# Kernel tuning notes

Hardware: AMD Instinct MI355X
Metric: run time of the kernel (lower is better)

Reference implementation:

```python
import jax, jax.numpy as jnp
import numpy as np

N_NODES = 100000
N_EDGES = 640000


def _sage_conv(x, src, dst, w_agg, b, w_root, n_nodes):
    # mean aggregation of source features into destination nodes
    msgs = x[src]  # [E, D] gather
    summed = jax.ops.segment_sum(msgs, dst, num_segments=n_nodes)  # [N, D]
    deg = jax.ops.segment_sum(jnp.ones((src.shape[0],), dtype=x.dtype), dst,
                              num_segments=n_nodes)  # [N]
    mean = summed / jnp.clip(deg, 1.0)[:, None]  # isolated nodes -> 0
    # PyG SAGEConv: lin_l(agg) + lin_r(x); bias lives on lin_l
    return mean @ w_agg.T + b + x @ w_root.T


def setup_inputs() -> dict:
    key = jax.random.key(0)
    ks = jax.random.split(key, 8)
    d_in, d_hid, d_out = 128, 256, 64
    x = jax.random.normal(ks[0], (N_NODES, d_in), dtype=jnp.float32)
    edge_index = jax.random.randint(ks[1], (2, N_EDGES), 0, N_NODES, dtype=jnp.int64)
    s = 0.05
    return {
        "x": x,
        "edge_index": edge_index,
        "w1_agg": jax.random.normal(ks[2], (d_hid, d_in), dtype=jnp.float32) * s,
        "b1": jax.random.normal(ks[3], (d_hid,), dtype=jnp.float32) * s,
        "w1_root": jax.random.normal(ks[4], (d_hid, d_in), dtype=jnp.float32) * s,
        "w2_agg": jax.random.normal(ks[5], (d_out, d_hid), dtype=jnp.float32) * s,
        "b2": jax.random.normal(ks[6], (d_out,), dtype=jnp.float32) * s,
        "w2_root": jax.random.normal(ks[7], (d_out, d_hid), dtype=jnp.float32) * s,
    }


def reference(x, edge_index, w1_agg, b1, w1_root, w2_agg, b2, w2_root):
    src, dst = edge_index[0], edge_index[1]
    n = x.shape[0]
    h = _sage_conv(x, src, dst, w1_agg, b1, w1_root, n)
    h = jax.nn.relu(h)
    # dropout(p=0.5) is identity in eval mode
    h = _sage_conv(h, src, dst, w2_agg, b2, w2_root, n)
    return jax.nn.log_softmax(h, axis=1)
```

## Files before the change

### kernel.cpp

```cpp
#include <hip/hip_runtime.h>

#define N_NODES 100000
#define N_EDGES 640000
#define D_IN 128
#define D_HID 256
#define D_OUT 64

#define NROWPAD 100096
#define CAP 32

#define OB_CNT      0u
#define OB_BUCKET   401408u
#define OB_XQ       13201408u
#define OB_MEANQ    26013696u
#define OB_HB       38825984u
#define OB_ZRB      90075136u
#define OB_ZAQ      102887424u
#define OB_WCAT1    109293568u
#define OB_WCAT2    109424640u

typedef __attribute__((ext_vector_type(8))) short bf16x8;
typedef __attribute__((ext_vector_type(4))) float f32x4;
typedef __attribute__((ext_vector_type(2))) float f32x2;

__device__ __forceinline__ ushort f2bf(float f) {
    uint u = __float_as_uint(f);
    u += 0x7FFFu + ((u >> 16) & 1u);
    return (ushort)(u >> 16);
}
__device__ __forceinline__ float bf1(ushort u) { return __uint_as_float((uint)u << 16); }
__device__ __forceinline__ uchar f2q(float v) {
    return (uchar)(__builtin_amdgcn_cvt_pk_fp8_f32(v, v, 0, false) & 0xFF);
}
__device__ __forceinline__ uint pk8(float4 v) {
    uint q = (uint)__builtin_amdgcn_cvt_pk_fp8_f32(v.x, v.y, 0, false);
    return (uint)__builtin_amdgcn_cvt_pk_fp8_f32(v.z, v.w, (int)q, true);
}
__device__ __forceinline__ uint pkbf(float lo, float hi) {
    return (__float_as_uint(lo) >> 16) | (__float_as_uint(hi) & 0xFFFF0000u);
}


__global__ __launch_bounds__(256) void k_z(
    int* __restrict__ cnt,
    const float* __restrict__ w1a, const float* __restrict__ w1r,
    const float* __restrict__ w2r, const float* __restrict__ w2a,
    ushort* __restrict__ wcat1, ushort* __restrict__ wcat2)
{
    int b = blockIdx.x;
    if (b < 98) {
        int i = (b * 256 + threadIdx.x) * 4;
        *(int4*)(cnt + i) = make_int4(0, 0, 0, 0);
    } else {
        int i = (b - 98) * 256 + threadIdx.x;
        if (i < 65536) {
            int n = i >> 8, k = i & 255;
            float v = (k < 128) ? w1a[n * 128 + k] : w1r[n * 128 + (k - 128)];
            wcat1[i] = f2bf(v);
        } else {
            int j = i - 65536;
            int n = j >> 8, k = j & 255;
            float v = (n < 64) ? w2r[n * 256 + k] : w2a[(n - 64) * 256 + k];
            wcat2[j] = f2bf(v);
        }
    }
}


__global__ __launch_bounds__(256) void k_fc(
    const int* __restrict__ src, const int* __restrict__ dst,
    int* __restrict__ cnt, int* __restrict__ bucket,
    const float* __restrict__ x, uchar* __restrict__ xq)
{
    int b = blockIdx.x;
    int tid = threadIdx.x;

    if (b < 625) {
        int e = (b * 256 + tid) * 4;
        int4 d = *(const int4*)(dst + e);
        int4 sv = *(const int4*)(src + e);
        int p0 = atomicAdd(&cnt[d.x], 1);
        int p1 = atomicAdd(&cnt[d.y], 1);
        int p2 = atomicAdd(&cnt[d.z], 1);
        int p3 = atomicAdd(&cnt[d.w], 1);

        size_t i = ((size_t)b * 256 + tid) * 16;
        float4 v0 = *(const float4*)(x + i);
        float4 v1 = *(const float4*)(x + i + 4);
        float4 v2 = *(const float4*)(x + i + 8);
        float4 v3 = *(const float4*)(x + i + 12);
        uint4 q;
        q.x = pk8(v0); q.y = pk8(v1); q.z = pk8(v2); q.w = pk8(v3);
        *(uint4*)(xq + i) = q;

        if (p0 < CAP) bucket[(d.x << 5) + p0] = sv.x;
        if (p1 < CAP) bucket[(d.y << 5) + p1] = sv.y;
        if (p2 < CAP) bucket[(d.z << 5) + p2] = sv.z;
        if (p3 < CAP) bucket[(d.w << 5) + p3] = sv.w;
    } else {
        size_t i = ((size_t)b * 256 + tid) * 16;
        float4 v0 = *(const float4*)(x + i);
        float4 v1 = *(const float4*)(x + i + 4);
        float4 v2 = *(const float4*)(x + i + 8);
        float4 v3 = *(const float4*)(x + i + 12);
        uint4 q;
        q.x = pk8(v0); q.y = pk8(v1); q.z = pk8(v2); q.w = pk8(v3);
        *(uint4*)(xq + i) = q;
    }
}


__global__ __launch_bounds__(256) void k_gather(
    const uchar* __restrict__ xq, const int* __restrict__ cnt,
    const int* __restrict__ bucket, uchar* __restrict__ meanq)
{
    int tid = threadIdx.x;
    int node = blockIdx.x * 8 + (tid >> 5);
    int l = tid & 31;
    int g = l & 3, t = l >> 2;
    int nraw = cnt[node];
    int n = min(nraw, CAP);
    const int* cs = bucket + (node << 5);

    float a[16] = {};
    for (int j = 0; j < n; j += 4) {
        int jj = j + g;
        int ii = (jj < n) ? jj : 0;
        float w = (jj < n) ? 1.0f : 0.0f;
        int s = cs[ii];
        uint4 q = *(const uint4*)(xq + (size_t)s * D_IN + t * 16);
        f32x2 p;
        p = __builtin_amdgcn_cvt_pk_f32_fp8(q.x, false); a[0] += w*p.x; a[1] += w*p.y;
        p = __builtin_amdgcn_cvt_pk_f32_fp8(q.x, true);  a[2] += w*p.x; a[3] += w*p.y;
        p = __builtin_amdgcn_cvt_pk_f32_fp8(q.y, false); a[4] += w*p.x; a[5] += w*p.y;
        p = __builtin_amdgcn_cvt_pk_f32_fp8(q.y, true);  a[6] += w*p.x; a[7] += w*p.y;
        p = __builtin_amdgcn_cvt_pk_f32_fp8(q.z, false); a[8] += w*p.x; a[9] += w*p.y;
        p = __builtin_amdgcn_cvt_pk_f32_fp8(q.z, true);  a[10]+= w*p.x; a[11]+= w*p.y;
        p = __builtin_amdgcn_cvt_pk_f32_fp8(q.w, false); a[12]+= w*p.x; a[13]+= w*p.y;
        p = __builtin_amdgcn_cvt_pk_f32_fp8(q.w, true);  a[14]+= w*p.x; a[15]+= w*p.y;
    }

    float b[8];
    #pragma unroll
    for (int j = 0; j < 8; ++j) {
        int base = (j & 3) + 8 * (j >> 2);
        float mine = (l & 1) ? a[base + 4] : a[base];
        float send = (l & 1) ? a[base]     : a[base + 4];
        b[j] = mine + __shfl_xor(send, 1);
    }
    float c[4];
    #pragma unroll
    for (int j = 0; j < 4; ++j) {
        float mine = (l & 2) ? b[j + 4] : b[j];
        float send = (l & 2) ? b[j]     : b[j + 4];
        c[j] = mine + __shfl_xor(send, 2);
    }
    float id = 1.0f / fmaxf((float)nraw, 1.0f);
    uint q = (uint)__builtin_amdgcn_cvt_pk_fp8_f32(c[0] * id, c[1] * id, 0, false);
    q = (uint)__builtin_amdgcn_cvt_pk_fp8_f32(c[2] * id, c[3] * id, (int)q, true);
    *(uint*)(meanq + (size_t)node * D_IN + t * 16 + (l & 3) * 4) = q;
}


template<int MODE>
__global__ __launch_bounds__(256, 2) void k_gemm(
    const void* __restrict__ A0v, const void* __restrict__ A1v,
    const ushort* __restrict__ B,
    const float* __restrict__ bias,
    void* __restrict__ out0, void* __restrict__ out1)
{
    __shared__ char lds[32 * 1024];
    const int BB = (MODE == 0) ? 8192 : 16384;

    const int tid = threadIdx.x;
    const int lane = tid & 63;
    const int w = tid >> 6;
    const int wm = w >> 1, wn = w & 1;
    const int row0 = blockIdx.x * 128;
    const int col0 = blockIdx.y * 128;

    f32x4 acc[4][4] = {};

    for (int kt = 0; kt < 4; ++kt) {
        const int k0 = kt * 64;

        if (MODE == 0) {
            const uchar* asrc = (kt < 2) ? (const uchar*)A0v : (const uchar*)A1v;
            int kbyte = (kt & 1) * 64;
            #pragma unroll
            for (int i = 0; i < 2; ++i) {
                int elem = i * 256 + tid;
                int r = elem >> 2;
                int c4 = (elem & 3) ^ (r & 3);
                const uchar* gp = asrc + (size_t)(row0 + r) * 128 + kbyte + c4 * 16;
                __builtin_amdgcn_global_load_lds(
                    (const __attribute__((address_space(1))) void*)gp,
                    (__attribute__((address_space(3))) void*)&lds[i * 4096 + w * 1024],
                    16, 0, 0);
            }
        } else {
            const ushort* asrc = (const ushort*)A0v;
            #pragma unroll
            for (int i = 0; i < 4; ++i) {
                int elem = i * 256 + tid;
                int r = elem >> 3;
                int c8 = (elem & 7) ^ (r & 7);
                const ushort* gp = asrc + (size_t)(row0 + r) * 256 + k0 + c8 * 8;
                __builtin_amdgcn_global_load_lds(
                    (const __attribute__((address_space(1))) void*)gp,
                    (__attribute__((address_space(3))) void*)&lds[i * 4096 + w * 1024],
                    16, 0, 0);
            }
        }
        #pragma unroll
        for (int i = 0; i < 4; ++i) {
            int elem = i * 256 + tid;
            int r = elem >> 3;
            int c8 = (elem & 7) ^ (r & 7);
            const ushort* gp = B + (size_t)(col0 + r) * 256 + k0 + c8 * 8;
            __builtin_amdgcn_global_load_lds(
                (const __attribute__((address_space(1))) void*)gp,
                (__attribute__((address_space(3))) void*)&lds[BB + i * 4096 + w * 1024],
                16, 0, 0);
        }
        asm volatile("s_waitcnt vmcnt(0)" ::: "memory");
        __syncthreads();

        #pragma unroll
        for (int ks = 0; ks < 2; ++ks) {
            bf16x8 af[4], bfr[4];
            #pragma unroll
            for (int mi = 0; mi < 4; ++mi) {
                int r = wm * 64 + mi * 16 + (lane & 15);
                int g = lane >> 4;
                if (MODE == 0) {
                    int c4l = ks * 2 + (g >> 1);
                    int abyte = r * 64 + ((c4l ^ (r & 3)) << 4) + ((g & 1) << 3);
                    uint2 q = *(const uint2*)(lds + abyte);
                    f32x2 p0 = __builtin_amdgcn_cvt_pk_f32_fp8(q.x, false);
                    f32x2 p1 = __builtin_amdgcn_cvt_pk_f32_fp8(q.x, true);
                    f32x2 p2 = __builtin_amdgcn_cvt_pk_f32_fp8(q.y, false);
                    f32x2 p3 = __builtin_amdgcn_cvt_pk_f32_fp8(q.y, true);
                    uint4 u;
                    u.x = pkbf(p0.x, p0.y); u.y = pkbf(p1.x, p1.y);
                    u.z = pkbf(p2.x, p2.y); u.w = pkbf(p3.x, p3.y);
                    af[mi] = *(bf16x8*)&u;
                } else {
                    int c8 = ks * 4 + g;
                    int abyte = r * 128 + ((c8 ^ (r & 7)) << 4);
                    af[mi] = *(const bf16x8*)(lds + abyte);
                }
            }
            #pragma unroll
            for (int ni = 0; ni < 4; ++ni) {
                int r = wn * 64 + ni * 16 + (lane & 15);
                int c8 = ks * 4 + (lane >> 4);
                int byteoff = BB + r * 128 + ((c8 ^ (r & 7)) << 4);
                bfr[ni] = *(const bf16x8*)(lds + byteoff);
            }
            #pragma unroll
            for (int mi = 0; mi < 4; ++mi)
                #pragma unroll
                for (int ni = 0; ni < 4; ++ni)
                    acc[mi][ni] = __builtin_amdgcn_mfma_f32_16x16x32_bf16(
                        af[mi], bfr[ni], acc[mi][ni], 0, 0, 0);
        }
        __syncthreads();
    }

    const int orow_base = row0 + wm * 64;
    const int ocol_base = col0 + wn * 64;
    #pragma unroll
    for (int mi = 0; mi < 4; ++mi) {
        #pragma unroll
        for (int ni = 0; ni < 4; ++ni) {
            int ocol = ocol_base + ni * 16 + (lane & 15);
            #pragma unroll
            for (int r = 0; r < 4; ++r) {
                int orow = orow_base + mi * 16 + (lane >> 4) * 4 + r;
                float v = acc[mi][ni][r];
                if (MODE == 0) {
                    v = fmaxf(v + bias[ocol], 0.0f);
                    ((ushort*)out0)[(size_t)orow * 256 + ocol] = f2bf(v);
                } else {
                    if (ocol < 64)
                        ((ushort*)out0)[(size_t)orow * 64 + ocol] = f2bf(v + bias[ocol]);
                    else
                        ((uchar*)out1)[(size_t)orow * 64 + (ocol - 64)] = f2q(v);
                }
            }
        }
    }
}


__global__ __launch_bounds__(256) void k_final(
    const ushort* __restrict__ zrb, const uchar* __restrict__ zaq,
    const int* __restrict__ cnt, const int* __restrict__ bucket,
    float* __restrict__ out)
{
    int tid = threadIdx.x;
    int lane = tid & 63;
    int l = lane & 31;
    int node = blockIdx.x * 8 + (tid >> 5);
    int g = l & 7, t = l >> 3;
    int nraw = cnt[node];
    int n = min(nraw, CAP);
    const int* cs = bucket + (node << 5);

    float a[16] = {};
    for (int j = 0; j < n; j += 8) {
        int jj = j + g;
        int ii = (jj < n) ? jj : 0;
        float w = (jj < n) ? 1.0f : 0.0f;
        int s = cs[ii];
        uint4 q = *(const uint4*)(zaq + (size_t)s * 64 + t * 16);
        f32x2 p;
        p = __builtin_amdgcn_cvt_pk_f32_fp8(q.x, false); a[0] += w*p.x; a[1] += w*p.y;
        p = __builtin_amdgcn_cvt_pk_f32_fp8(q.x, true);  a[2] += w*p.x; a[3] += w*p.y;
        p = __builtin_amdgcn_cvt_pk_f32_fp8(q.y, false); a[4] += w*p.x; a[5] += w*p.y;
        p = __builtin_amdgcn_cvt_pk_f32_fp8(q.y, true);  a[6] += w*p.x; a[7] += w*p.y;
        p = __builtin_amdgcn_cvt_pk_f32_fp8(q.z, false); a[8] += w*p.x; a[9] += w*p.y;
        p = __builtin_amdgcn_cvt_pk_f32_fp8(q.z, true);  a[10]+= w*p.x; a[11]+= w*p.y;
        p = __builtin_amdgcn_cvt_pk_f32_fp8(q.w, false); a[12]+= w*p.x; a[13]+= w*p.y;
        p = __builtin_amdgcn_cvt_pk_f32_fp8(q.w, true);  a[14]+= w*p.x; a[15]+= w*p.y;
    }

    float b[8];
    #pragma unroll
    for (int j = 0; j < 8; ++j) {
        float mine = (l & 1) ? a[2*j+1] : a[2*j];
        float send = (l & 1) ? a[2*j]   : a[2*j+1];
        b[j] = mine + __shfl_xor(send, 1);
    }
    float c[4];
    #pragma unroll
    for (int j = 0; j < 4; ++j) {
        float mine = (l & 2) ? b[2*j+1] : b[2*j];
        float send = (l & 2) ? b[2*j]   : b[2*j+1];
        c[j] = mine + __shfl_xor(send, 2);
    }
    float m0 = (l & 4) ? c[1] : c[0];
    float s0 = (l & 4) ? c[0] : c[1];
    float e0 = m0 + __shfl_xor(s0, 4);
    float m1 = (l & 4) ? c[3] : c[2];
    float s1 = (l & 4) ? c[2] : c[3];
    float e1 = m1 + __shfl_xor(s1, 4);

    int c0 = t * 16 + (l & 7);
    float id = 1.0f / fmaxf((float)nraw, 1.0f);
    float v0 = e0 * id + bf1(zrb[(size_t)node * 64 + c0]);
    float v1 = e1 * id + bf1(zrb[(size_t)node * 64 + c0 + 8]);

    float m = fmaxf(v0, v1);
    #pragma unroll
    for (int o = 1; o < 32; o <<= 1) m = fmaxf(m, __shfl_xor(m, o));
    float ssum = __expf(v0 - m) + __expf(v1 - m);
    #pragma unroll
    for (int o = 1; o < 32; o <<= 1) ssum += __shfl_xor(ssum, o);
    float lse = m + __logf(ssum);

    out[(size_t)node * 64 + c0]     = v0 - lse;
    out[(size_t)node * 64 + c0 + 8] = v1 - lse;
}


extern "C" void kernel_launch(void* const* d_in, const int* in_sizes, int n_in,
                              void* d_out, int out_size, void* d_ws, size_t ws_size,
                              hipStream_t stream)
{
    const float* x   = (const float*)d_in[0];
    const int*   ei  = (const int*)d_in[1];
    const float* w1a = (const float*)d_in[2];
    const float* b1  = (const float*)d_in[3];
    const float* w1r = (const float*)d_in[4];
    const float* w2a = (const float*)d_in[5];
    const float* b2  = (const float*)d_in[6];
    const float* w2r = (const float*)d_in[7];
    float* out = (float*)d_out;

    char* ws = (char*)d_ws;
    const int* src = ei;
    const int* dst = ei + N_EDGES;

    int*    cnt       = (int*)(ws + OB_CNT);
    int*    bucket    = (int*)(ws + OB_BUCKET);
    uchar*  xq        = (uchar*)(ws + OB_XQ);
    uchar*  meanq     = (uchar*)(ws + OB_MEANQ);
    ushort* hb        = (ushort*)(ws + OB_HB);
    ushort* zrb       = (ushort*)(ws + OB_ZRB);
    uchar*  zaq       = (uchar*)(ws + OB_ZAQ);
    ushort* wcat1     = (ushort*)(ws + OB_WCAT1);
    ushort* wcat2     = (ushort*)(ws + OB_WCAT2);

    k_z<<<482, 256, 0, stream>>>(cnt, w1a, w1r, w2r, w2a, wcat1, wcat2);
    k_fc<<<3125, 256, 0, stream>>>(src, dst, cnt, bucket, x, xq);

    k_gather<<<12500, 256, 0, stream>>>(xq, cnt, bucket, meanq);

    dim3 g1(NROWPAD / 128, 2);
    k_gemm<0><<<g1, 256, 0, stream>>>((const void*)meanq, (const void*)xq,
                                      wcat1, b1, (void*)hb, nullptr);

    dim3 g2(NROWPAD / 128, 1);
    k_gemm<1><<<g2, 256, 0, stream>>>((const void*)hb, (const void*)hb,
                                      wcat2, b2, (void*)zrb, (void*)zaq);

    k_final<<<12500, 256, 0, stream>>>(zrb, zaq, cnt, bucket, out);
}
```

Before: 145.0 us.

## Fuse neighbor mean gather into first-layer GEMM via LDS staging

The separate gather kernel that wrote the FP8 neighbor mean to global memory is folded into the first GEMM. Each 512-thread block now gathers means for its 128 rows straight into swizzled LDS, then runs the full 256-column GEMM with the root features streamed from xq. This drops the meanq write and re-read and one kernel launch. In exchange the gather phase runs with far fewer, LDS-heavy blocks (56 KB each), which may lower occupancy and latency hiding for the random-access neighbor loads. The second GEMM is de-templated into a dedicated kernel with no functional change.

```diff
diff --git a/kernel.cpp b/kernel.cpp
--- a/kernel.cpp
+++ b/kernel.cpp
@@ -12,7 +12,6 @@
 #define OB_CNT      0u
 #define OB_BUCKET   401408u
 #define OB_XQ       13201408u
-#define OB_MEANQ    26013696u
 #define OB_HB       38825984u
 #define OB_ZRB      90075136u
 #define OB_ZAQ      102887424u
@@ -110,117 +109,192 @@
 }
 
 
-__global__ __launch_bounds__(256) void k_gather(
+__global__ __launch_bounds__(512) void k_g1(
     const uchar* __restrict__ xq, const int* __restrict__ cnt,
-    const int* __restrict__ bucket, uchar* __restrict__ meanq)
-{
-    int tid = threadIdx.x;
-    int node = blockIdx.x * 8 + (tid >> 5);
-    int l = tid & 31;
-    int g = l & 3, t = l >> 2;
-    int nraw = cnt[node];
-    int n = min(nraw, CAP);
-    const int* cs = bucket + (node << 5);
-
-    float a[16] = {};
-    for (int j = 0; j < n; j += 4) {
-        int jj = j + g;
-        int ii = (jj < n) ? jj : 0;
-        float w = (jj < n) ? 1.0f : 0.0f;
-        int s = cs[ii];
-        uint4 q = *(const uint4*)(xq + (size_t)s * D_IN + t * 16);
-        f32x2 p;
-        p = __builtin_amdgcn_cvt_pk_f32_fp8(q.x, false); a[0] += w*p.x; a[1] += w*p.y;
-        p = __builtin_amdgcn_cvt_pk_f32_fp8(q.x, true);  a[2] += w*p.x; a[3] += w*p.y;
-        p = __builtin_amdgcn_cvt_pk_f32_fp8(q.y, false); a[4] += w*p.x; a[5] += w*p.y;
-        p = __builtin_amdgcn_cvt_pk_f32_fp8(q.y, true);  a[6] += w*p.x; a[7] += w*p.y;
-        p = __builtin_amdgcn_cvt_pk_f32_fp8(q.z, false); a[8] += w*p.x; a[9] += w*p.y;
-        p = __builtin_amdgcn_cvt_pk_f32_fp8(q.z, true);  a[10]+= w*p.x; a[11]+= w*p.y;
-        p = __builtin_amdgcn_cvt_pk_f32_fp8(q.w, false); a[12]+= w*p.x; a[13]+= w*p.y;
-        p = __builtin_amdgcn_cvt_pk_f32_fp8(q.w, true);  a[14]+= w*p.x; a[15]+= w*p.y;
-    }
-
-    float b[8];
-    #pragma unroll
-    for (int j = 0; j < 8; ++j) {
-        int base = (j & 3) + 8 * (j >> 2);
-        float mine = (l & 1) ? a[base + 4] : a[base];
-        float send = (l & 1) ? a[base]     : a[base + 4];
-        b[j] = mine + __shfl_xor(send, 1);
-    }
-    float c[4];
-    #pragma unroll
-    for (int j = 0; j < 4; ++j) {
-        float mine = (l & 2) ? b[j + 4] : b[j];
-        float send = (l & 2) ? b[j]     : b[j + 4];
-        c[j] = mine + __shfl_xor(send, 2);
-    }
-    float id = 1.0f / fmaxf((float)nraw, 1.0f);
-    uint q = (uint)__builtin_amdgcn_cvt_pk_fp8_f32(c[0] * id, c[1] * id, 0, false);
-    q = (uint)__builtin_amdgcn_cvt_pk_fp8_f32(c[2] * id, c[3] * id, (int)q, true);
-    *(uint*)(meanq + (size_t)node * D_IN + t * 16 + (l & 3) * 4) = q;
-}
-
-
-template<int MODE>
-__global__ __launch_bounds__(256, 2) void k_gemm(
-    const void* __restrict__ A0v, const void* __restrict__ A1v,
-    const ushort* __restrict__ B,
-    const float* __restrict__ bias,
-    void* __restrict__ out0, void* __restrict__ out1)
+    const int* __restrict__ bucket, const ushort* __restrict__ wcat1,
+    const float* __restrict__ b1, ushort* __restrict__ hb)
+{
+    __shared__ char lds[57344];
+
+    const int tid = threadIdx.x;
+    const int row0 = blockIdx.x * 128;
+    const int lane = tid & 63;
+    const int w = tid >> 6;
+    const int wm = w >> 2, wn = w & 3;
+
+    {
+        int l = tid & 31;
+        int hw = tid >> 5;
+        int g = l & 3, t = l >> 2;
+        for (int it = 0; it < 8; ++it) {
+            int rloc = it * 16 + hw;
+            int node = row0 + rloc;
+            int nraw = cnt[node];
+            int n = min(nraw, CAP);
+            const int* cs = bucket + (node << 5);
+
+            float a[16] = {};
+            for (int j = 0; j < n; j += 4) {
+                int jj = j + g;
+                int ii = (jj < n) ? jj : 0;
+                float wgt = (jj < n) ? 1.0f : 0.0f;
+                int s = cs[ii];
+                uint4 q = *(const uint4*)(xq + (size_t)s * D_IN + t * 16);
+                f32x2 p;
+                p = __builtin_amdgcn_cvt_pk_f32_fp8(q.x, false); a[0] += wgt*p.x; a[1] += wgt*p.y;
+                p = __builtin_amdgcn_cvt_pk_f32_fp8(q.x, true);  a[2] += wgt*p.x; a[3] += wgt*p.y;
+                p = __builtin_amdgcn_cvt_pk_f32_fp8(q.y, false); a[4] += wgt*p.x; a[5] += wgt*p.y;
+                p = __builtin_amdgcn_cvt_pk_f32_fp8(q.y, true);  a[6] += wgt*p.x; a[7] += wgt*p.y;
+                p = __builtin_amdgcn_cvt_pk_f32_fp8(q.z, false); a[8] += wgt*p.x; a[9] += wgt*p.y;
+                p = __builtin_amdgcn_cvt_pk_f32_fp8(q.z, true);  a[10]+= wgt*p.x; a[11]+= wgt*p.y;
+                p = __builtin_amdgcn_cvt_pk_f32_fp8(q.w, false); a[12]+= wgt*p.x; a[13]+= wgt*p.y;
+                p = __builtin_amdgcn_cvt_pk_f32_fp8(q.w, true);  a[14]+= wgt*p.x; a[15]+= wgt*p.y;
+            }
+            float bb[8];
+            #pragma unroll
+            for (int j = 0; j < 8; ++j) {
+                int base = (j & 3) + 8 * (j >> 2);
+                float mine = (l & 1) ? a[base + 4] : a[base];
+                float send = (l & 1) ? a[base]     : a[base + 4];
+                bb[j] = mine + __shfl_xor(send, 1);
+            }
+            float c[4];
+            #pragma unroll
+            for (int j = 0; j < 4; ++j) {
+                float mine = (l & 2) ? bb[j + 4] : bb[j];
+                float send = (l & 2) ? bb[j]     : bb[j + 4];
+                c[j] = mine + __shfl_xor(send, 2);
+            }
+            float id = 1.0f / fmaxf((float)nraw, 1.0f);
+            uint q = (uint)__builtin_amdgcn_cvt_pk_fp8_f32(c[0]*id, c[1]*id, 0, false);
+            q = (uint)__builtin_amdgcn_cvt_pk_fp8_f32(c[2]*id, c[3]*id, (int)q, true);
+            *(uint*)(lds + rloc * 128 + ((t ^ (rloc & 7)) << 4) + (l & 3) * 4) = q;
+        }
+    }
+    __syncthreads();
+
+    f32x4 acc[4][4] = {};
+
+    for (int kt = 0; kt < 4; ++kt) {
+        if (kt >= 2) {
+            int r = tid >> 2;
+            int c4 = (tid & 3) ^ (r & 3);
+            const uchar* gp = xq + (size_t)(row0 + r) * 128 + (kt & 1) * 64 + c4 * 16;
+            __builtin_amdgcn_global_load_lds(
+                (const __attribute__((address_space(1))) void*)gp,
+                (__attribute__((address_space(3))) void*)&lds[16384 + w * 1024],
+                16, 0, 0);
+        }
+        #pragma unroll
+        for (int i = 0; i < 4; ++i) {
+            int elem = i * 512 + tid;
+            int r = elem >> 3;
+            int c8 = (elem & 7) ^ (r & 7);
+            const ushort* gp = wcat1 + (size_t)r * 256 + kt * 64 + c8 * 8;
+            __builtin_amdgcn_global_load_lds(
+                (const __attribute__((address_space(1))) void*)gp,
+                (__attribute__((address_space(3))) void*)&lds[24576 + i * 8192 + w * 1024],
+                16, 0, 0);
+        }
+        asm volatile("s_waitcnt vmcnt(0)" ::: "memory");
+        __syncthreads();
+
+        #pragma unroll
+        for (int ks = 0; ks < 2; ++ks) {
+            bf16x8 af[4], bfr[4];
+            #pragma unroll
+            for (int mi = 0; mi < 4; ++mi) {
+                int r = wm * 64 + mi * 16 + (lane & 15);
+                int g = lane >> 4;
+                int c4l = ks * 2 + (g >> 1);
+                int abyte;
+                if (kt < 2) {
+                    int ct = kt * 4 + c4l;
+                    abyte = r * 128 + ((ct ^ (r & 7)) << 4) + ((g & 1) << 3);
+                } else {
+                    abyte = 16384 + r * 64 + ((c4l ^ (r & 3)) << 4) + ((g & 1) << 3);
+                }
+                uint2 q = *(const uint2*)(lds + abyte);
+                f32x2 p0 = __builtin_amdgcn_cvt_pk_f32_fp8(q.x, false);
+                f32x2 p1 = __builtin_amdgcn_cvt_pk_f32_fp8(q.x, true);
+                f32x2 p2 = __builtin_amdgcn_cvt_pk_f32_fp8(q.y, false);
+                f32x2 p3 = __builtin_amdgcn_cvt_pk_f32_fp8(q.y, true);
+                uint4 u;
+                u.x = pkbf(p0.x, p0.y); u.y = pkbf(p1.x, p1.y);
+                u.z = pkbf(p2.x, p2.y); u.w = pkbf(p3.x, p3.y);
+                af[mi] = *(bf16x8*)&u;
+            }
+            #pragma unroll
+            for (int ni = 0; ni < 4; ++ni) {
+                int r = wn * 64 + ni * 16 + (lane & 15);
+                int c8 = ks * 4 + (lane >> 4);
+                bfr[ni] = *(const bf16x8*)(lds + 24576 + r * 128 + ((c8 ^ (r & 7)) << 4));
+            }
+            #pragma unroll
+            for (int mi = 0; mi < 4; ++mi)
+                #pragma unroll
+                for (int ni = 0; ni < 4; ++ni)
+                    acc[mi][ni] = __builtin_amdgcn_mfma_f32_16x16x32_bf16(
+                        af[mi], bfr[ni], acc[mi][ni], 0, 0, 0);
+        }
+        __syncthreads();
+    }
+
+    const int orow_base = row0 + wm * 64;
+    const int ocol_base = wn * 64;
+    #pragma unroll
+    for (int mi = 0; mi < 4; ++mi) {
+        #pragma unroll
+        for (int ni = 0; ni < 4; ++ni) {
+            int ocol = ocol_base + ni * 16 + (lane & 15);
+            #pragma unroll
+            for (int r = 0; r < 4; ++r) {
+                int orow = orow_base + mi * 16 + (lane >> 4) * 4 + r;
+                float v = fmaxf(acc[mi][ni][r] + b1[ocol], 0.0f);
+                hb[(size_t)orow * 256 + ocol] = f2bf(v);
+            }
+        }
+    }
+}
+
+
+__global__ __launch_bounds__(256, 2) void k_gemm2(
+    const ushort* __restrict__ hb, const ushort* __restrict__ B,
+    const float* __restrict__ b2,
+    ushort* __restrict__ zrb, uchar* __restrict__ zaq)
 {
     __shared__ char lds[32 * 1024];
-    const int BB = (MODE == 0) ? 8192 : 16384;
 
     const int tid = threadIdx.x;
     const int lane = tid & 63;
     const int w = tid >> 6;
     const int wm = w >> 1, wn = w & 1;
     const int row0 = blockIdx.x * 128;
-    const int col0 = blockIdx.y * 128;
 
     f32x4 acc[4][4] = {};
 
     for (int kt = 0; kt < 4; ++kt) {
         const int k0 = kt * 64;
-
-        if (MODE == 0) {
-            const uchar* asrc = (kt < 2) ? (const uchar*)A0v : (const uchar*)A1v;
-            int kbyte = (kt & 1) * 64;
-            #pragma unroll
-            for (int i = 0; i < 2; ++i) {
-                int elem = i * 256 + tid;
-                int r = elem >> 2;
-                int c4 = (elem & 3) ^ (r & 3);
-                const uchar* gp = asrc + (size_t)(row0 + r) * 128 + kbyte + c4 * 16;
-                __builtin_amdgcn_global_load_lds(
-                    (const __attribute__((address_space(1))) void*)gp,
-                    (__attribute__((address_space(3))) void*)&lds[i * 4096 + w * 1024],
-                    16, 0, 0);
-            }
-        } else {
-            const ushort* asrc = (const ushort*)A0v;
-            #pragma unroll
-            for (int i = 0; i < 4; ++i) {
-                int elem = i * 256 + tid;
-                int r = elem >> 3;
-                int c8 = (elem & 7) ^ (r & 7);
-                const ushort* gp = asrc + (size_t)(row0 + r) * 256 + k0 + c8 * 8;
-                __builtin_amdgcn_global_load_lds(
-                    (const __attribute__((address_space(1))) void*)gp,
-                    (__attribute__((address_space(3))) void*)&lds[i * 4096 + w * 1024],
-                    16, 0, 0);
-            }
-        }
         #pragma unroll
         for (int i = 0; i < 4; ++i) {
             int elem = i * 256 + tid;
             int r = elem >> 3;
             int c8 = (elem & 7) ^ (r & 7);
-            const ushort* gp = B + (size_t)(col0 + r) * 256 + k0 + c8 * 8;
+            const ushort* gp = hb + (size_t)(row0 + r) * 256 + k0 + c8 * 8;
             __builtin_amdgcn_global_load_lds(
                 (const __attribute__((address_space(1))) void*)gp,
-                (__attribute__((address_space(3))) void*)&lds[BB + i * 4096 + w * 1024],
+                (__attribute__((address_space(3))) void*)&lds[i * 4096 + w * 1024],
+                16, 0, 0);
+        }
+        #pragma unroll
+        for (int i = 0; i < 4; ++i) {
+            int elem = i * 256 + tid;
+            int r = elem >> 3;
+            int c8 = (elem & 7) ^ (r & 7);
+            const ushort* gp = B + (size_t)r * 256 + k0 + c8 * 8;
+            __builtin_amdgcn_global_load_lds(
+                (const __attribute__((address_space(1))) void*)gp,
+                (__attribute__((address_space(3))) void*)&lds[16384 + i * 4096 + w * 1024],
                 16, 0, 0);
         }
         asm volatile("s_waitcnt vmcnt(0)" ::: "memory");
@@ -232,31 +306,14 @@
             #pragma unroll
             for (int mi = 0; mi < 4; ++mi) {
                 int r = wm * 64 + mi * 16 + (lane & 15);
-                int g = lane >> 4;
-                if (MODE == 0) {
-                    int c4l = ks * 2 + (g >> 1);
-                    int abyte = r * 64 + ((c4l ^ (r & 3)) << 4) + ((g & 1) << 3);
-                    uint2 q = *(const uint2*)(lds + abyte);
-                    f32x2 p0 = __builtin_amdgcn_cvt_pk_f32_fp8(q.x, false);
-                    f32x2 p1 = __builtin_amdgcn_cvt_pk_f32_fp8(q.x, true);
-                    f32x2 p2 = __builtin_amdgcn_cvt_pk_f32_fp8(q.y, false);
-                    f32x2 p3 = __builtin_amdgcn_cvt_pk_f32_fp8(q.y, true);
-                    uint4 u;
-                    u.x = pkbf(p0.x, p0.y); u.y = pkbf(p1.x, p1.y);
-                    u.z = pkbf(p2.x, p2.y); u.w = pkbf(p3.x, p3.y);
-                    af[mi] = *(bf16x8*)&u;
-                } else {
-                    int c8 = ks * 4 + g;
-                    int abyte = r * 128 + ((c8 ^ (r & 7)) << 4);
-                    af[mi] = *(const bf16x8*)(lds + abyte);
-                }
+                int c8 = ks * 4 + (lane >> 4);
+                af[mi] = *(const bf16x8*)(lds + r * 128 + ((c8 ^ (r & 7)) << 4));
             }
             #pragma unroll
             for (int ni = 0; ni < 4; ++ni) {
                 int r = wn * 64 + ni * 16 + (lane & 15);
                 int c8 = ks * 4 + (lane >> 4);
-                int byteoff = BB + r * 128 + ((c8 ^ (r & 7)) << 4);
-                bfr[ni] = *(const bf16x8*)(lds + byteoff);
+                bfr[ni] = *(const bf16x8*)(lds + 16384 + r * 128 + ((c8 ^ (r & 7)) << 4));
             }
             #pragma unroll
             for (int mi = 0; mi < 4; ++mi)
@@ -269,7 +326,7 @@
     }
 
     const int orow_base = row0 + wm * 64;
-    const int ocol_base = col0 + wn * 64;
+    const int ocol_base = wn * 64;
     #pragma unroll
     for (int mi = 0; mi < 4; ++mi) {
         #pragma unroll
@@ -279,15 +336,10 @@
             for (int r = 0; r < 4; ++r) {
                 int orow = orow_base + mi * 16 + (lane >> 4) * 4 + r;
                 float v = acc[mi][ni][r];
-                if (MODE == 0) {
-                    v = fmaxf(v + bias[ocol], 0.0f);
-                    ((ushort*)out0)[(size_t)orow * 256 + ocol] = f2bf(v);
-                } else {
-                    if (ocol < 64)
-                        ((ushort*)out0)[(size_t)orow * 64 + ocol] = f2bf(v + bias[ocol]);
-                    else
-                        ((uchar*)out1)[(size_t)orow * 64 + (ocol - 64)] = f2q(v);
-                }
+                if (ocol < 64)
+                    zrb[(size_t)orow * 64 + ocol] = f2bf(v + b2[ocol]);
+                else
+                    zaq[(size_t)orow * 64 + (ocol - 64)] = f2q(v);
             }
         }
     }
@@ -383,28 +435,20 @@
     const int* src = ei;
     const int* dst = ei + N_EDGES;
 
-    int*    cnt       = (int*)(ws + OB_CNT);
-    int*    bucket    = (int*)(ws + OB_BUCKET);
-    uchar*  xq        = (uchar*)(ws + OB_XQ);
-    uchar*  meanq     = (uchar*)(ws + OB_MEANQ);
-    ushort* hb        = (ushort*)(ws + OB_HB);
-    ushort* zrb       = (ushort*)(ws + OB_ZRB);
-    uchar*  zaq       = (uchar*)(ws + OB_ZAQ);
-    ushort* wcat1     = (ushort*)(ws + OB_WCAT1);
-    ushort* wcat2     = (ushort*)(ws + OB_WCAT2);
+    int*    cnt    = (int*)(ws + OB_CNT);
+    int*    bucket = (int*)(ws + OB_BUCKET);
+    uchar*  xq     = (uchar*)(ws + OB_XQ);
+    ushort* hb     = (ushort*)(ws + OB_HB);
+    ushort* zrb    = (ushort*)(ws + OB_ZRB);
+    uchar*  zaq    = (uchar*)(ws + OB_ZAQ);
+    ushort* wcat1  = (ushort*)(ws + OB_WCAT1);
+    ushort* wcat2  = (ushort*)(ws + OB_WCAT2);
 
     k_z<<<482, 256, 0, stream>>>(cnt, w1a, w1r, w2r, w2a, wcat1, wcat2);
     k_fc<<<3125, 256, 0, stream>>>(src, dst, cnt, bucket, x, xq);
 
-    k_gather<<<12500, 256, 0, stream>>>(xq, cnt, bucket, meanq);
-
-    dim3 g1(NROWPAD / 128, 2);
-    k_gemm<0><<<g1, 256, 0, stream>>>((const void*)meanq, (const void*)xq,
-                                      wcat1, b1, (void*)hb, nullptr);
-
-    dim3 g2(NROWPAD / 128, 1);
-    k_gemm<1><<<g2, 256, 0, stream>>>((const void*)hb, (const void*)hb,
-                                      wcat2, b2, (void*)zrb, (void*)zaq);
+    k_g1<<<NROWPAD / 128, 512, 0, stream>>>(xq, cnt, bucket, wcat1, b1, hb);
+    k_gemm2<<<NROWPAD / 128, 256, 0, stream>>>(hb, wcat2, b2, zrb, zaq);
 
     k_final<<<12500, 256, 0, stream>>>(zrb, zaq, cnt, bucket, out);
 }
```

New measurement: 190.5 us. +31.4%, slower.
